# Performance work log

Hardware: AMD Instinct MI355X
Metric: run time of the kernel (lower is better)

## Reference

```python
import jax, jax.numpy as jnp
import numpy as np

B = 2
N_FINE = 100000
N_COARSE = 25000
H = 128
IN_DIM = 2 * H + 1  # 257


def setup_inputs() -> dict:
    key = jax.random.key(0)
    ks = jax.random.split(key, 10)
    s_in = 1.0 / np.sqrt(IN_DIM)
    s_h = 1.0 / np.sqrt(H)
    return {
        "x": jax.random.normal(ks[0], (B, N_COARSE, H), dtype=jnp.float32),
        "x_scale": jax.random.normal(ks[1], (B, N_FINE, H), dtype=jnp.float32),
        "fine2coarse_index": jax.random.randint(ks[2], (N_FINE,), 0, N_COARSE),
        "distances": jax.random.uniform(ks[3], (1, N_FINE, 1), dtype=jnp.float32),
        "W1": jax.random.uniform(ks[4], (IN_DIM, H), minval=-s_in, maxval=s_in, dtype=jnp.float32),
        "b1": jax.random.uniform(ks[5], (H,), minval=-s_in, maxval=s_in, dtype=jnp.float32),
        "W2": jax.random.uniform(ks[6], (H, H), minval=-s_h, maxval=s_h, dtype=jnp.float32),
        "b2": jax.random.uniform(ks[7], (H,), minval=-s_h, maxval=s_h, dtype=jnp.float32),
        "W3": jax.random.uniform(ks[8], (H, H), minval=-s_h, maxval=s_h, dtype=jnp.float32),
        "b3": jax.random.uniform(ks[9], (H,), minval=-s_h, maxval=s_h, dtype=jnp.float32),
    }


def reference(x, x_scale, fine2coarse_index, distances, W1, b1, W2, b2, W3, b3):
    # gather coarse features to fine nodes: [B, N_fine, H]
    xg = jnp.take(x, fine2coarse_index, axis=1)
    d = jnp.broadcast_to(distances, (xg.shape[0], xg.shape[1], 1))
    h = jnp.concatenate([xg, x_scale, d], axis=2)  # [B, N_fine, 2H+1]
    # MLP: Linear -> SiLU -> Linear -> SiLU -> Linear
    h = jax.nn.silu(h @ W1 + b1)
    h = jax.nn.silu(h @ W2 + b2)
    return h @ W3 + b3
```

## Files before the change

kernel.cpp:

```cpp
#include <hip/hip_runtime.h>
#include <math.h>

#define H 128
#define NF 100000
#define NC 25000
#define TM 64

typedef _Float16 f16;
typedef f16 f16x8 __attribute__((ext_vector_type(8)));
typedef f16 f16x4 __attribute__((ext_vector_type(4)));
typedef float f32x4 __attribute__((ext_vector_type(4)));

#define MFMA16(a, b, c) __builtin_amdgcn_mfma_f32_16x16x32_f16((a), (b), (c), 0, 0, 0)


__global__ void prep_w(const float* __restrict__ W1, const float* __restrict__ W2,
                       const float* __restrict__ W3, f16* __restrict__ ws)
{
    int i = blockIdx.x * 256 + threadIdx.x;
    if (i < 32768) {
        int j = i & 7, lane = (i >> 3) & 63, kk = (i >> 9) & 7, nt = i >> 12;
        int n = nt * 16 + (lane & 15);
        int k = kk * 32 + (lane >> 4) * 8 + j;
        ws[i] = (f16)W1[k * H + n];
    } else if (i < 49152) {
        int q = i - 32768;
        int j = q & 7, lane = (q >> 3) & 63, kk = (q >> 9) & 3, nt = q >> 11;
        int n = nt * 16 + (lane & 15);
        int k = kk * 32 + (lane >> 4) * 8 + j;
        ws[i] = (f16)W2[k * H + n];
    } else {
        int q = i - 49152;
        int j = q & 7, lane = (q >> 3) & 63, kk = (q >> 9) & 3, nt = q >> 11;
        int n = nt * 16 + (lane & 15);
        int k = kk * 32 + (lane >> 4) * 8 + j;
        ws[i] = (f16)W3[k * H + n];
    }
}

__device__ __forceinline__ float silu_f(float v) {
    return v / (1.0f + __expf(-v));
}

__global__ __launch_bounds__(256, 4)
void fused_mlp_v11(const float* __restrict__ x,
                   const float* __restrict__ xsc,
                   const int*   __restrict__ f2c,
                   const float* __restrict__ dist,
                   const float* __restrict__ W1,
                   const float* __restrict__ b1,
                   const float* __restrict__ b2,
                   const float* __restrict__ b3,
                   const f16*   __restrict__ ws,
                   float* __restrict__ out)
{
    __shared__ __align__(16) f16 sA[TM * H];
    __shared__ float sD[TM];
    __shared__ int   sCI[TM];

    const int t = threadIdx.x;
    const int l = t & 63, w = t >> 6;
    const int wRow = (w >> 1) * 32;
    const int wnt  = (w & 1) * 4;
    const int lr = l & 15, lg = l >> 4;
    const int R0 = blockIdx.x * TM;

    if (t < TM) {
        int Rs = R0 + t;
        int bb = Rs >= NF;
        int nn = Rs - bb * NF;
        sCI[t] = bb * NC + f2c[nn];
        sD[t]  = dist[nn];
    }
    __syncthreads();

    const f16* F1 = ws;
    const f16* F2 = ws + 32768;
    const f16* F3 = ws + 49152;

    f32x4 acc[2][4];
    #pragma unroll
    for (int nt = 0; nt < 4; ++nt) {
        int col = (wnt + nt) * 16 + lr;
        float bc = b1[col];
        float wc = W1[256 * H + col];
        #pragma unroll
        for (int mt = 0; mt < 2; ++mt)
            #pragma unroll
            for (int r = 0; r < 4; ++r)
                acc[mt][nt][r] = bc + sD[wRow + mt * 16 + lg * 4 + r] * wc;
    }

    #pragma unroll
    for (int i = 0; i < 8; ++i) {
        int f = i * 256 + t;
        int row = f >> 5, col = (f & 31) * 4;
        float4 v = *(const float4*)(x + (long long)sCI[row] * H + col);
        f16x4 hv; hv[0] = (f16)v.x; hv[1] = (f16)v.y; hv[2] = (f16)v.z; hv[3] = (f16)v.w;
        *(f16x4*)(sA + row * H + (((col >> 3) ^ (row & 7)) << 3) + (col & 7)) = hv;
    }
    __syncthreads();

    {
        f16x8 wv[4][4];
        #pragma unroll
        for (int kk = 0; kk < 4; ++kk)
            #pragma unroll
            for (int nt = 0; nt < 4; ++nt)
                wv[kk][nt] = *(const f16x8*)(F1 + ((((wnt + nt) * 8 + kk) * 64 + l) << 3));
        #pragma unroll
        for (int kk = 0; kk < 4; ++kk) {
            int k = kk * 32 + (lg << 3);
            int slot = (((k >> 3) ^ (lr & 7)) << 3);
            f16x8 a0 = *(const f16x8*)(sA + (wRow + lr) * H + slot);
            f16x8 a1 = *(const f16x8*)(sA + (wRow + 16 + lr) * H + slot);
            #pragma unroll
            for (int nt = 0; nt < 4; ++nt) {
                acc[0][nt] = MFMA16(a0, wv[kk][nt], acc[0][nt]);
                acc[1][nt] = MFMA16(a1, wv[kk][nt], acc[1][nt]);
            }
        }
    }
    __syncthreads();

    #pragma unroll
    for (int i = 0; i < 8; ++i) {
        int f = i * 256 + t;
        int row = f >> 5, col = (f & 31) * 4;
        float4 v = *(const float4*)(xsc + (long long)(R0 + row) * H + col);
        f16x4 hv; hv[0] = (f16)v.x; hv[1] = (f16)v.y; hv[2] = (f16)v.z; hv[3] = (f16)v.w;
        *(f16x4*)(sA + row * H + (((col >> 3) ^ (row & 7)) << 3) + (col & 7)) = hv;
    }
    __syncthreads();

    {
        f16x8 wv[4][4];
        #pragma unroll
        for (int kk = 0; kk < 4; ++kk)
            #pragma unroll
            for (int nt = 0; nt < 4; ++nt)
                wv[kk][nt] = *(const f16x8*)(F1 + ((((wnt + nt) * 8 + kk + 4) * 64 + l) << 3));
        #pragma unroll
        for (int kk = 0; kk < 4; ++kk) {
            int k = kk * 32 + (lg << 3);
            int slot = (((k >> 3) ^ (lr & 7)) << 3);
            f16x8 a0 = *(const f16x8*)(sA + (wRow + lr) * H + slot);
            f16x8 a1 = *(const f16x8*)(sA + (wRow + 16 + lr) * H + slot);
            #pragma unroll
            for (int nt = 0; nt < 4; ++nt) {
                acc[0][nt] = MFMA16(a0, wv[kk][nt], acc[0][nt]);
                acc[1][nt] = MFMA16(a1, wv[kk][nt], acc[1][nt]);
            }
        }
    }
    __syncthreads();

    #pragma unroll
    for (int nt = 0; nt < 4; ++nt)
        #pragma unroll
        for (int mt = 0; mt < 2; ++mt)
            #pragma unroll
            for (int r = 0; r < 4; ++r) {
                int row = wRow + mt * 16 + lg * 4 + r;
                int col = (wnt + nt) * 16 + lr;
                sA[row * H + (((col >> 3) ^ (row & 7)) << 3) + (col & 7)] =
                    (f16)silu_f(acc[mt][nt][r]);
            }
    __syncthreads();

    #pragma unroll
    for (int nt = 0; nt < 4; ++nt) {
        float bc = b2[(wnt + nt) * 16 + lr];
        #pragma unroll
        for (int mt = 0; mt < 2; ++mt)
            #pragma unroll
            for (int r = 0; r < 4; ++r)
                acc[mt][nt][r] = bc;
    }
    {
        f16x8 wv[4][4];
        #pragma unroll
        for (int kk = 0; kk < 4; ++kk)
            #pragma unroll
            for (int nt = 0; nt < 4; ++nt)
                wv[kk][nt] = *(const f16x8*)(F2 + ((((wnt + nt) * 4 + kk) * 64 + l) << 3));
        #pragma unroll
        for (int kk = 0; kk < 4; ++kk) {
            int k = kk * 32 + (lg << 3);
            int slot = (((k >> 3) ^ (lr & 7)) << 3);
            f16x8 a0 = *(const f16x8*)(sA + (wRow + lr) * H + slot);
            f16x8 a1 = *(const f16x8*)(sA + (wRow + 16 + lr) * H + slot);
            #pragma unroll
            for (int nt = 0; nt < 4; ++nt) {
                acc[0][nt] = MFMA16(a0, wv[kk][nt], acc[0][nt]);
                acc[1][nt] = MFMA16(a1, wv[kk][nt], acc[1][nt]);
            }
        }
    }
    __syncthreads();

    #pragma unroll
    for (int nt = 0; nt < 4; ++nt)
        #pragma unroll
        for (int mt = 0; mt < 2; ++mt)
            #pragma unroll
            for (int r = 0; r < 4; ++r) {
                int row = wRow + mt * 16 + lg * 4 + r;
                int col = (wnt + nt) * 16 + lr;
                sA[row * H + (((col >> 3) ^ (row & 7)) << 3) + (col & 7)] =
                    (f16)silu_f(acc[mt][nt][r]);
            }
    __syncthreads();

    #pragma unroll
    for (int nt = 0; nt < 4; ++nt) {
        float bc = b3[(wnt + nt) * 16 + lr];
        #pragma unroll
        for (int mt = 0; mt < 2; ++mt)
            #pragma unroll
            for (int r = 0; r < 4; ++r)
                acc[mt][nt][r] = bc;
    }
    {
        f16x8 wv[4][4];
        #pragma unroll
        for (int kk = 0; kk < 4; ++kk)
            #pragma unroll
            for (int nt = 0; nt < 4; ++nt)
                wv[kk][nt] = *(const f16x8*)(F3 + ((((wnt + nt) * 4 + kk) * 64 + l) << 3));
        #pragma unroll
        for (int kk = 0; kk < 4; ++kk) {
            int k = kk * 32 + (lg << 3);
            int slot = (((k >> 3) ^ (lr & 7)) << 3);
            f16x8 a0 = *(const f16x8*)(sA + (wRow + lr) * H + slot);
            f16x8 a1 = *(const f16x8*)(sA + (wRow + 16 + lr) * H + slot);
            #pragma unroll
            for (int nt = 0; nt < 4; ++nt) {
                acc[0][nt] = MFMA16(a0, wv[kk][nt], acc[0][nt]);
                acc[1][nt] = MFMA16(a1, wv[kk][nt], acc[1][nt]);
            }
        }
    }

    #pragma unroll
    for (int mt = 0; mt < 2; ++mt)
        #pragma unroll
        for (int nt = 0; nt < 4; ++nt)
            #pragma unroll
            for (int r = 0; r < 4; ++r) {
                long long row = (long long)R0 + wRow + mt * 16 + lg * 4 + r;
                int col = (wnt + nt) * 16 + lr;
                out[row * H + col] = acc[mt][nt][r];
            }
}

extern "C" void kernel_launch(void* const* d_in, const int* in_sizes, int n_in,
                              void* d_out, int out_size, void* d_ws, size_t ws_size,
                              hipStream_t stream)
{
    const float* x    = (const float*)d_in[0];
    const float* xsc  = (const float*)d_in[1];
    const int*   f2c  = (const int*)d_in[2];
    const float* dist = (const float*)d_in[3];
    const float* W1   = (const float*)d_in[4];
    const float* b1   = (const float*)d_in[5];
    const float* W2   = (const float*)d_in[6];
    const float* b2   = (const float*)d_in[7];
    const float* W3   = (const float*)d_in[8];
    const float* b3   = (const float*)d_in[9];
    f16* ws = (f16*)d_ws;

    prep_w<<<256, 256, 0, stream>>>(W1, W2, W3, ws);

    const int n_rows = 2 * NF;
    dim3 grid(n_rows / TM);
    fused_mlp_v11<<<grid, 256, 0, stream>>>(x, xsc, f2c, dist, W1, b1, b2, b3,
                                            ws, (float*)d_out);
}
```

Before: 76.95 us.

## Load layer-1 inputs directly into MFMA registers, skipping LDS staging

Layer 1 now reads the gathered coarse features and the fine-scale features straight from global memory into MFMA A-fragments, converting them to fp16 in registers. This removes the LDS staging stores, the per-block index and distance tables, and several __syncthreads. Weight fragments are also loaded per MFMA instead of being prefetched as 16-register arrays, which lowers register pressure but exposes global load latency. Each lane now issues 32-byte scattered row reads instead of the earlier coalesced cooperative loads, which may reduce memory efficiency.

```diff
diff --git a/kernel.cpp b/kernel.cpp
--- a/kernel.cpp
+++ b/kernel.cpp
@@ -42,8 +42,15 @@
     return v / (1.0f + __expf(-v));
 }
 
+__device__ __forceinline__ f16x8 cvt8(float4 v0, float4 v1) {
+    f16x8 r;
+    r[0] = (f16)v0.x; r[1] = (f16)v0.y; r[2] = (f16)v0.z; r[3] = (f16)v0.w;
+    r[4] = (f16)v1.x; r[5] = (f16)v1.y; r[6] = (f16)v1.z; r[7] = (f16)v1.w;
+    return r;
+}
+
 __global__ __launch_bounds__(256, 4)
-void fused_mlp_v11(const float* __restrict__ x,
+void fused_mlp_v12(const float* __restrict__ x,
                    const float* __restrict__ xsc,
                    const int*   __restrict__ f2c,
                    const float* __restrict__ dist,
@@ -55,8 +62,6 @@
                    float* __restrict__ out)
 {
     __shared__ __align__(16) f16 sA[TM * H];
-    __shared__ float sD[TM];
-    __shared__ int   sCI[TM];
 
     const int t = threadIdx.x;
     const int l = t & 63, w = t >> 6;
@@ -65,20 +70,29 @@
     const int lr = l & 15, lg = l >> 4;
     const int R0 = blockIdx.x * TM;
 
-    if (t < TM) {
-        int Rs = R0 + t;
-        int bb = Rs >= NF;
-        int nn = Rs - bb * NF;
-        sCI[t] = bb * NC + f2c[nn];
-        sD[t]  = dist[nn];
-    }
-    __syncthreads();
-
     const f16* F1 = ws;
     const f16* F2 = ws + 32768;
     const f16* F3 = ws + 49152;
 
+    const int row0 = R0 + wRow + lr;
+    const int row1 = row0 + 16;
+    const int bb0 = row0 >= NF, bb1 = row1 >= NF;
+    const int ci0 = f2c[row0 - bb0 * NF];
+    const int ci1 = f2c[row1 - bb1 * NF];
+    const float* xg0 = x + (long long)(bb0 * NC + ci0) * H;
+    const float* xg1 = x + (long long)(bb1 * NC + ci1) * H;
+    const float* xs0 = xsc + (long long)row0 * H;
+    const float* xs1 = xsc + (long long)row1 * H;
+
     f32x4 acc[2][4];
+    float dd[2][4];
+    #pragma unroll
+    for (int mt = 0; mt < 2; ++mt) {
+        int r4 = R0 + wRow + mt * 16 + lg * 4;
+        int bb = r4 >= NF;
+        float4 dv = *(const float4*)(dist + (r4 - bb * NF));
+        dd[mt][0] = dv.x; dd[mt][1] = dv.y; dd[mt][2] = dv.z; dd[mt][3] = dv.w;
+    }
     #pragma unroll
     for (int nt = 0; nt < 4; ++nt) {
         int col = (wnt + nt) * 16 + lr;
@@ -88,72 +102,37 @@
         for (int mt = 0; mt < 2; ++mt)
             #pragma unroll
             for (int r = 0; r < 4; ++r)
-                acc[mt][nt][r] = bc + sD[wRow + mt * 16 + lg * 4 + r] * wc;
-    }
-
-    #pragma unroll
-    for (int i = 0; i < 8; ++i) {
-        int f = i * 256 + t;
-        int row = f >> 5, col = (f & 31) * 4;
-        float4 v = *(const float4*)(x + (long long)sCI[row] * H + col);
-        f16x4 hv; hv[0] = (f16)v.x; hv[1] = (f16)v.y; hv[2] = (f16)v.z; hv[3] = (f16)v.w;
-        *(f16x4*)(sA + row * H + (((col >> 3) ^ (row & 7)) << 3) + (col & 7)) = hv;
-    }
-    __syncthreads();
-
-    {
-        f16x8 wv[4][4];
-        #pragma unroll
-        for (int kk = 0; kk < 4; ++kk)
-            #pragma unroll
-            for (int nt = 0; nt < 4; ++nt)
-                wv[kk][nt] = *(const f16x8*)(F1 + ((((wnt + nt) * 8 + kk) * 64 + l) << 3));
-        #pragma unroll
-        for (int kk = 0; kk < 4; ++kk) {
-            int k = kk * 32 + (lg << 3);
-            int slot = (((k >> 3) ^ (lr & 7)) << 3);
-            f16x8 a0 = *(const f16x8*)(sA + (wRow + lr) * H + slot);
-            f16x8 a1 = *(const f16x8*)(sA + (wRow + 16 + lr) * H + slot);
-            #pragma unroll
-            for (int nt = 0; nt < 4; ++nt) {
-                acc[0][nt] = MFMA16(a0, wv[kk][nt], acc[0][nt]);
-                acc[1][nt] = MFMA16(a1, wv[kk][nt], acc[1][nt]);
-            }
-        }
-    }
-    __syncthreads();
-
-    #pragma unroll
-    for (int i = 0; i < 8; ++i) {
-        int f = i * 256 + t;
-        int row = f >> 5, col = (f & 31) * 4;
-        float4 v = *(const float4*)(xsc + (long long)(R0 + row) * H + col);
-        f16x4 hv; hv[0] = (f16)v.x; hv[1] = (f16)v.y; hv[2] = (f16)v.z; hv[3] = (f16)v.w;
-        *(f16x4*)(sA + row * H + (((col >> 3) ^ (row & 7)) << 3) + (col & 7)) = hv;
-    }
-    __syncthreads();
-
-    {
-        f16x8 wv[4][4];
-        #pragma unroll
-        for (int kk = 0; kk < 4; ++kk)
-            #pragma unroll
-            for (int nt = 0; nt < 4; ++nt)
-                wv[kk][nt] = *(const f16x8*)(F1 + ((((wnt + nt) * 8 + kk + 4) * 64 + l) << 3));
-        #pragma unroll
-        for (int kk = 0; kk < 4; ++kk) {
-            int k = kk * 32 + (lg << 3);
-            int slot = (((k >> 3) ^ (lr & 7)) << 3);
-            f16x8 a0 = *(const f16x8*)(sA + (wRow + lr) * H + slot);
-            f16x8 a1 = *(const f16x8*)(sA + (wRow + 16 + lr) * H + slot);
-            #pragma unroll
-            for (int nt = 0; nt < 4; ++nt) {
-                acc[0][nt] = MFMA16(a0, wv[kk][nt], acc[0][nt]);
-                acc[1][nt] = MFMA16(a1, wv[kk][nt], acc[1][nt]);
-            }
-        }
-    }
-    __syncthreads();
+                acc[mt][nt][r] = bc + dd[mt][r] * wc;
+    }
+
+    {
+        #pragma unroll
+        for (int kk = 0; kk < 4; ++kk) {
+            const int kc = kk * 32 + (lg << 3);
+            f16x8 a0 = cvt8(*(const float4*)(xg0 + kc), *(const float4*)(xg0 + kc + 4));
+            f16x8 a1 = cvt8(*(const float4*)(xg1 + kc), *(const float4*)(xg1 + kc + 4));
+            #pragma unroll
+            for (int nt = 0; nt < 4; ++nt) {
+                f16x8 wv = *(const f16x8*)(F1 + ((((wnt + nt) * 8 + kk) * 64 + l) << 3));
+                acc[0][nt] = MFMA16(a0, wv, acc[0][nt]);
+                acc[1][nt] = MFMA16(a1, wv, acc[1][nt]);
+            }
+        }
+    }
+    {
+        #pragma unroll
+        for (int kk = 0; kk < 4; ++kk) {
+            const int kc = kk * 32 + (lg << 3);
+            f16x8 a0 = cvt8(*(const float4*)(xs0 + kc), *(const float4*)(xs0 + kc + 4));
+            f16x8 a1 = cvt8(*(const float4*)(xs1 + kc), *(const float4*)(xs1 + kc + 4));
+            #pragma unroll
+            for (int nt = 0; nt < 4; ++nt) {
+                f16x8 wv = *(const f16x8*)(F1 + ((((wnt + nt) * 8 + kk + 4) * 64 + l) << 3));
+                acc[0][nt] = MFMA16(a0, wv, acc[0][nt]);
+                acc[1][nt] = MFMA16(a1, wv, acc[1][nt]);
+            }
+        }
+    }
 
     #pragma unroll
     for (int nt = 0; nt < 4; ++nt)
@@ -178,12 +157,6 @@
                 acc[mt][nt][r] = bc;
     }
     {
-        f16x8 wv[4][4];
-        #pragma unroll
-        for (int kk = 0; kk < 4; ++kk)
-            #pragma unroll
-            for (int nt = 0; nt < 4; ++nt)
-                wv[kk][nt] = *(const f16x8*)(F2 + ((((wnt + nt) * 4 + kk) * 64 + l) << 3));
         #pragma unroll
         for (int kk = 0; kk < 4; ++kk) {
             int k = kk * 32 + (lg << 3);
@@ -192,8 +165,9 @@
             f16x8 a1 = *(const f16x8*)(sA + (wRow + 16 + lr) * H + slot);
             #pragma unroll
             for (int nt = 0; nt < 4; ++nt) {
-                acc[0][nt] = MFMA16(a0, wv[kk][nt], acc[0][nt]);
-                acc[1][nt] = MFMA16(a1, wv[kk][nt], acc[1][nt]);
+                f16x8 wv = *(const f16x8*)(F2 + ((((wnt + nt) * 4 + kk) * 64 + l) << 3));
+                acc[0][nt] = MFMA16(a0, wv, acc[0][nt]);
+                acc[1][nt] = MFMA16(a1, wv, acc[1][nt]);
             }
         }
     }
@@ -222,12 +196,6 @@
                 acc[mt][nt][r] = bc;
     }
     {
-        f16x8 wv[4][4];
-        #pragma unroll
-        for (int kk = 0; kk < 4; ++kk)
-            #pragma unroll
-            for (int nt = 0; nt < 4; ++nt)
-                wv[kk][nt] = *(const f16x8*)(F3 + ((((wnt + nt) * 4 + kk) * 64 + l) << 3));
         #pragma unroll
         for (int kk = 0; kk < 4; ++kk) {
             int k = kk * 32 + (lg << 3);
@@ -236,8 +204,9 @@
             f16x8 a1 = *(const f16x8*)(sA + (wRow + 16 + lr) * H + slot);
             #pragma unroll
             for (int nt = 0; nt < 4; ++nt) {
-                acc[0][nt] = MFMA16(a0, wv[kk][nt], acc[0][nt]);
-                acc[1][nt] = MFMA16(a1, wv[kk][nt], acc[1][nt]);
+                f16x8 wv = *(const f16x8*)(F3 + ((((wnt + nt) * 4 + kk) * 64 + l) << 3));
+                acc[0][nt] = MFMA16(a0, wv, acc[0][nt]);
+                acc[1][nt] = MFMA16(a1, wv, acc[1][nt]);
             }
         }
     }
@@ -274,6 +243,6 @@
 
     const int n_rows = 2 * NF;
     dim3 grid(n_rows / TM);
-    fused_mlp_v11<<<grid, 256, 0, stream>>>(x, xsc, f2c, dist, W1, b1, b2, b3,
+    fused_mlp_v12<<<grid, 256, 0, stream>>>(x, xsc, f2c, dist, W1, b1, b2, b3,
                                             ws, (float*)d_out);
 }
```

Measured after the change: 99.10 us. +28.8%, slower.
